# Kernel optimization log

Measured on AMD Instinct MI355X. Metric: run time of the kernel, lower is better.

## Reference

```python
import jax, jax.numpy as jnp
import numpy as np

B, S, D_IN, D_OUT = 4, 2048, 1024, 64
USE_MASK = True

def setup_inputs() -> dict:
    key = jax.random.key(0)
    ks = jax.random.split(key, 6)
    return {
        "inputs_for_keys": jax.random.normal(ks[0], (B, S, D_IN), jnp.float32),
        "inputs_for_values": jax.random.normal(ks[1], (B, S, D_IN), jnp.float32),
        "inputs_for_queries": jax.random.normal(ks[2], (B, S, D_IN), jnp.float32),
        "Weight_Q": jax.random.normal(ks[3], (D_IN, D_OUT), jnp.float32) * 0.02,
        "Weight_K": jax.random.normal(ks[4], (D_IN, D_OUT), jnp.float32) * 0.02,
        "Weight_V": jax.random.normal(ks[5], (D_IN, D_OUT), jnp.float32) * 0.02,
    }

def reference(inputs_for_keys, inputs_for_values, inputs_for_queries, Weight_Q, Weight_K, Weight_V):
    Q = jnp.einsum('bsd,de->bse', inputs_for_queries, Weight_Q)
    K = jnp.einsum('bsd,de->bse', inputs_for_keys, Weight_K)
    V = jnp.einsum('bsd,de->bse', inputs_for_values, Weight_V)
    # scores: [B, S_q, S_k], scaled by sqrt(d_out)
    scores = jnp.einsum('bqe,bke->bqk', Q, K) / np.sqrt(D_OUT).astype(np.float32)
    if USE_MASK:
        # -inf strictly above the diagonal (causal mask), matching
        # transpose(tril(ones*-inf, -1)) in the original.
        q_idx = jnp.arange(S)[:, None]
        k_idx = jnp.arange(S)[None, :]
        scores = jnp.where(k_idx > q_idx, -jnp.inf, scores)
    attn = jax.nn.softmax(scores, axis=-1)
    return jnp.einsum('bqk,bke->bqe', attn, V)
```

## Files before the change

### kernel.cpp

```cpp
#include <hip/hip_runtime.h>
#include <hip/hip_bf16.h>
#include <stdint.h>

typedef __bf16 bf16_t;
typedef __bf16 bf16x8 __attribute__((ext_vector_type(8)));
typedef float f32x4 __attribute__((ext_vector_type(4)));

#define L2E 1.44269504088896340736f

static __device__ __forceinline__ f32x4 mfma16(bf16x8 a, bf16x8 b, f32x4 c) {
  return __builtin_amdgcn_mfma_f32_16x16x32_bf16(a, b, c, 0, 0, 0);
}

__global__ __launch_bounds__(256) void wt_kernel(const float* __restrict__ Wq,
                                                 const float* __restrict__ Wk,
                                                 const float* __restrict__ Wv,
                                                 bf16_t* __restrict__ Wt) {
  int gid = blockIdx.x * 256 + threadIdx.x;
  int proj = gid >> 16;
  int rem = gid & 65535;
  int k = rem >> 6, n = rem & 63;
  const float* W = (proj == 0) ? Wq : (proj == 1) ? Wk : Wv;
  float v = W[rem];
  if (proj == 0) v *= 0.125f;
  Wt[proj * 65536 + n * 1024 + k] = (bf16_t)v;
}

__global__ __launch_bounds__(256, 4) void proj_kernel(
    const float* __restrict__ Xq, const float* __restrict__ Xk, const float* __restrict__ Xv,
    const bf16_t* __restrict__ Wt,
    bf16_t* __restrict__ Qb, bf16_t* __restrict__ Kb, bf16_t* __restrict__ Vt) {
  __shared__ float Msm[4][16][68];
  __shared__ bf16_t Vsm[16][68];

  int tid = threadIdx.x;
  int w = tid >> 6, lane = tid & 63;
  int l15 = lane & 15, g = lane >> 4;
  int bid = blockIdx.x;
  int p = bid >> 9, t = bid & 511;
  int m0 = t * 16;
  const float* X = (p == 0) ? Xq : (p == 1) ? Xk : Xv;

  const float* xk = X + (size_t)(m0 + l15) * 1024 + w * 256 + g * 8;
  const bf16_t* wrow = Wt + p * 65536 + l15 * 1024 + w * 256 + g * 8;

  f32x4 acc[4] = {};

  float4 a0x = *(const float4*)xk;
  float4 a0y = *(const float4*)(xk + 4);
  bf16x8 w0[4], w1[4];
#pragma unroll
  for (int ct = 0; ct < 4; ++ct) w0[ct] = *(const bf16x8*)(wrow + ct * 16384);

  float4 a1x, a1y;
#pragma unroll
  for (int ks = 0; ks < 8; ++ks) {
    if (ks < 7) {
      const float* xn = xk + (ks + 1) * 32;
      a1x = *(const float4*)xn;
      a1y = *(const float4*)(xn + 4);
#pragma unroll
      for (int ct = 0; ct < 4; ++ct)
        w1[ct] = *(const bf16x8*)(wrow + ct * 16384 + (ks + 1) * 32);
    }
    bf16x8 af;
    af[0] = (bf16_t)a0x.x; af[1] = (bf16_t)a0x.y; af[2] = (bf16_t)a0x.z; af[3] = (bf16_t)a0x.w;
    af[4] = (bf16_t)a0y.x; af[5] = (bf16_t)a0y.y; af[6] = (bf16_t)a0y.z; af[7] = (bf16_t)a0y.w;
#pragma unroll
    for (int ct = 0; ct < 4; ++ct) acc[ct] = mfma16(af, w0[ct], acc[ct]);
    a0x = a1x; a0y = a1y;
#pragma unroll
    for (int ct = 0; ct < 4; ++ct) w0[ct] = w1[ct];
  }

#pragma unroll
  for (int ct = 0; ct < 4; ++ct)
#pragma unroll
    for (int r = 0; r < 4; ++r)
      Msm[w][g * 4 + r][ct * 16 + l15] = acc[ct][r];
  __syncthreads();

  int row = tid >> 4, c0 = (tid & 15) * 4;
  f32x4 s = *(const f32x4*)&Msm[0][row][c0];
#pragma unroll
  for (int w2 = 1; w2 < 4; ++w2) {
    f32x4 q = *(const f32x4*)&Msm[w2][row][c0];
    s[0] += q[0]; s[1] += q[1]; s[2] += q[2]; s[3] += q[3];
  }

  if (p < 2) {
    bf16_t* Ob = (p == 0) ? Qb : Kb;
    bf16_t o4[4] = {(bf16_t)s[0], (bf16_t)s[1], (bf16_t)s[2], (bf16_t)s[3]};
    *(uint2*)&Ob[(size_t)(m0 + row) * 64 + c0] = *(const uint2*)o4;
  } else {
#pragma unroll
    for (int i = 0; i < 4; ++i) Vsm[row][c0 + i] = (bf16_t)s[i];
    __syncthreads();
    if (tid < 128) {
      int d = tid >> 1, h = tid & 1;
      int b = t >> 7;
      int s_ = (t & 127) * 16 + h * 8;
      bf16_t tmp[8];
#pragma unroll
      for (int i = 0; i < 8; ++i) tmp[i] = Vsm[h * 8 + i][d];
      *(uint4*)(Vt + ((size_t)(b * 64 + d)) * 2048 + s_) = *(const uint4*)tmp;
    }
  }
}

#define NW 8
__global__ __launch_bounds__(512) void attn_kernel(
    const bf16_t* __restrict__ Qb, const bf16_t* __restrict__ Kb,
    const bf16_t* __restrict__ Vt, float* __restrict__ Out) {
  __shared__ alignas(16) char Psm[NW * 4096];
  __shared__ float accL[NW][32][64];
  __shared__ float mL[NW][32];
  __shared__ float lL[NW][32];

  int b = blockIdx.y;
  int x = blockIdx.x;
  int qt = (b >= 2) ? (63 - x) : x;
  int q0 = qt * 32;
  int tid = threadIdx.x;
  int w = tid >> 6, lane = tid & 63;
  int l15 = lane & 15, g = lane >> 4;
  char* Pw = Psm + w * 4096;

  bf16x8 qf[2][2];
#pragma unroll
  for (int h = 0; h < 2; ++h) {
    size_t qrow = (size_t)(b * 2048 + q0 + h * 16 + l15) * 64;
    qf[h][0] = *(const bf16x8*)(Qb + qrow + g * 8);
    qf[h][1] = *(const bf16x8*)(Qb + qrow + 32 + g * 8);
  }

  float m_run[2][4], l_run[2][4];
  f32x4 acc_o[2][4] = {};
#pragma unroll
  for (int h = 0; h < 2; ++h)
#pragma unroll
    for (int r = 0; r < 4; ++r) { m_run[h][r] = -1e30f; l_run[h][r] = 0.f; }

  int ntiles = (q0 + 95) >> 6;
  const bf16_t* kbase = Kb + (size_t)b * 2048 * 64;
  const bf16_t* vbase = Vt + (size_t)b * 64 * 2048;

  for (int t = w; t < ntiles; t += NW) {
    int kv0 = t * 64;
    f32x4 s[2][4] = {};
#pragma unroll
    for (int ct = 0; ct < 4; ++ct) {
      const bf16_t* kr = kbase + (size_t)(kv0 + ct * 16 + l15) * 64 + g * 8;
      bf16x8 kf0 = *(const bf16x8*)kr;
      bf16x8 kf1 = *(const bf16x8*)(kr + 32);
#pragma unroll
      for (int h = 0; h < 2; ++h) {
        s[h][ct] = mfma16(qf[h][0], kf0, s[h][ct]);
        s[h][ct] = mfma16(qf[h][1], kf1, s[h][ct]);
      }
    }
    if (t == ntiles - 1) {
#pragma unroll
      for (int h = 0; h < 2; ++h)
#pragma unroll
        for (int ct = 0; ct < 4; ++ct)
#pragma unroll
          for (int r = 0; r < 4; ++r) {
            int kg_ = kv0 + ct * 16 + l15;
            int qg_ = q0 + h * 16 + g * 4 + r;
            if (kg_ > qg_) s[h][ct][r] = -1e30f;
          }
    }

#pragma unroll
    for (int h = 0; h < 2; ++h)
#pragma unroll
      for (int r = 0; r < 4; ++r) {
        float mx = fmaxf(fmaxf(s[h][0][r], s[h][1][r]), fmaxf(s[h][2][r], s[h][3][r]));
        mx = fmaxf(mx, __shfl_xor(mx, 1, 64));
        mx = fmaxf(mx, __shfl_xor(mx, 2, 64));
        mx = fmaxf(mx, __shfl_xor(mx, 4, 64));
        mx = fmaxf(mx, __shfl_xor(mx, 8, 64));
        float mnew = fmaxf(m_run[h][r], mx);
        float scale = exp2f((m_run[h][r] - mnew) * L2E);
        m_run[h][r] = mnew;
        float ps = 0.f;
        int qrl = h * 16 + g * 4 + r;
        char* pb = Pw + qrl * 128;
        int swp = (qrl & 7) << 4;
#pragma unroll
        for (int ct = 0; ct < 4; ++ct) {
          float p = exp2f((s[h][ct][r] - mnew) * L2E);
          ps += p;
          *(bf16_t*)(pb + ((ct * 32 + l15 * 2) ^ swp)) = (bf16_t)p;
        }
        ps += __shfl_xor(ps, 1, 64);
        ps += __shfl_xor(ps, 2, 64);
        ps += __shfl_xor(ps, 4, 64);
        ps += __shfl_xor(ps, 8, 64);
        l_run[h][r] = l_run[h][r] * scale + ps;
#pragma unroll
        for (int dt = 0; dt < 4; ++dt) acc_o[h][dt][r] *= scale;
      }

    int swpr = (l15 & 7) << 4;
#pragma unroll
    for (int ks = 0; ks < 2; ++ks) {
      bf16x8 pf0 = *(const bf16x8*)(Pw + l15 * 128 + ((ks * 64 + g * 16) ^ swpr));
      bf16x8 pf1 = *(const bf16x8*)(Pw + (16 + l15) * 128 + ((ks * 64 + g * 16) ^ swpr));
#pragma unroll
      for (int dt = 0; dt < 4; ++dt) {
        const bf16_t* vr = vbase + (size_t)(dt * 16 + l15) * 2048 + kv0 + ks * 32 + g * 8;
        bf16x8 vf = *(const bf16x8*)vr;
        acc_o[0][dt] = mfma16(pf0, vf, acc_o[0][dt]);
        acc_o[1][dt] = mfma16(pf1, vf, acc_o[1][dt]);
      }
    }
  }

  if (l15 == 0) {
#pragma unroll
    for (int h = 0; h < 2; ++h)
#pragma unroll
      for (int r = 0; r < 4; ++r) {
        mL[w][h * 16 + g * 4 + r] = m_run[h][r];
        lL[w][h * 16 + g * 4 + r] = l_run[h][r];
      }
  }
#pragma unroll
  for (int h = 0; h < 2; ++h)
#pragma unroll
    for (int dt = 0; dt < 4; ++dt)
#pragma unroll
      for (int r = 0; r < 4; ++r)
        accL[w][h * 16 + g * 4 + r][dt * 16 + l15] = acc_o[h][dt][r];
  __syncthreads();

  int row = tid >> 4, c0 = (tid & 15) * 4;
  float M = -1e30f;
#pragma unroll
  for (int w2 = 0; w2 < NW; ++w2) M = fmaxf(M, mL[w2][row]);
  float L = 0.f;
  f32x4 o = {0.f, 0.f, 0.f, 0.f};
#pragma unroll
  for (int w2 = 0; w2 < NW; ++w2) {
    float sc = exp2f((mL[w2][row] - M) * L2E);
    L += lL[w2][row] * sc;
    f32x4 a = *(const f32x4*)&accL[w2][row][c0];
    o[0] += sc * a[0]; o[1] += sc * a[1]; o[2] += sc * a[2]; o[3] += sc * a[3];
  }
  float inv = 1.0f / L;
  float4 o4 = {o[0] * inv, o[1] * inv, o[2] * inv, o[3] * inv};
  *(float4*)&Out[(size_t)(b * 2048 + q0 + row) * 64 + c0] = o4;
}

extern "C" void kernel_launch(void* const* d_in, const int* in_sizes, int n_in,
                              void* d_out, int out_size, void* d_ws, size_t ws_size,
                              hipStream_t stream) {
  const float* Xk = (const float*)d_in[0];
  const float* Xv = (const float*)d_in[1];
  const float* Xq = (const float*)d_in[2];
  const float* Wq = (const float*)d_in[3];
  const float* Wk = (const float*)d_in[4];
  const float* Wv = (const float*)d_in[5];
  float* Out = (float*)d_out;

  bf16_t* ws = (bf16_t*)d_ws;
  bf16_t* Qb = ws;
  bf16_t* Kb = ws + 524288;
  bf16_t* Vt = ws + 1048576;
  bf16_t* Wt = ws + 1572864;

  wt_kernel<<<dim3(768), dim3(256), 0, stream>>>(Wq, Wk, Wv, Wt);
  proj_kernel<<<dim3(1536), dim3(256), 0, stream>>>(Xq, Xk, Xv, Wt, Qb, Kb, Vt);
  attn_kernel<<<dim3(64, 4), dim3(512), 0, stream>>>(Qb, Kb, Vt, Out);
}
```

Measured before the change: 65.63 us.

## Stage projection inputs into swizzled LDS via global_load_lds and preload weights

The projection kernel now copies each wave's 16x256 fp32 input slice into a 64KB shared buffer using direct global-to-LDS loads. Each row is read as fully contiguous 1KB segments, replacing the earlier strided per-lane 32-byte reads, and an XOR swizzle avoids bank conflicts when the data is read back from LDS. All weight fragments are loaded into registers up front, replacing the double-buffered software pipeline. The larger LDS footprint and register use cut the occupancy hint from 4 to 2 blocks, and a full vmcnt wait before the MFMA loop removes any overlap between loads and compute.

```diff
diff --git a/kernel.cpp b/kernel.cpp
--- a/kernel.cpp
+++ b/kernel.cpp
@@ -10,6 +10,12 @@
 
 static __device__ __forceinline__ f32x4 mfma16(bf16x8 a, bf16x8 b, f32x4 c) {
   return __builtin_amdgcn_mfma_f32_16x16x32_bf16(a, b, c, 0, 0, 0);
+}
+
+static __device__ __forceinline__ void gload_lds16(const void* g, void* l) {
+  __builtin_amdgcn_global_load_lds(
+      (const __attribute__((address_space(1))) uint32_t*)g,
+      (__attribute__((address_space(3))) uint32_t*)l, 16, 0, 0);
 }
 
 __global__ __launch_bounds__(256) void wt_kernel(const float* __restrict__ Wq,
@@ -26,12 +32,13 @@
   Wt[proj * 65536 + n * 1024 + k] = (bf16_t)v;
 }
 
-__global__ __launch_bounds__(256, 4) void proj_kernel(
+__global__ __launch_bounds__(256, 2) void proj_kernel(
     const float* __restrict__ Xq, const float* __restrict__ Xk, const float* __restrict__ Xv,
     const bf16_t* __restrict__ Wt,
     bf16_t* __restrict__ Qb, bf16_t* __restrict__ Kb, bf16_t* __restrict__ Vt) {
-  __shared__ float Msm[4][16][68];
-  __shared__ bf16_t Vsm[16][68];
+  __shared__ alignas(16) char Xs[65536];
+  float (*Msm)[16][68] = (float(*)[16][68])Xs;
+  bf16_t (*Vsm)[68] = (bf16_t(*)[68])(Xs + 18432);
 
   int tid = threadIdx.x;
   int w = tid >> 6, lane = tid & 63;
@@ -40,39 +47,42 @@
   int p = bid >> 9, t = bid & 511;
   int m0 = t * 16;
   const float* X = (p == 0) ? Xq : (p == 1) ? Xk : Xv;
-
-  const float* xk = X + (size_t)(m0 + l15) * 1024 + w * 256 + g * 8;
+  const char* xb = (const char*)X + (size_t)m0 * 4096;
+  char* Xw = Xs + w * 16384;
+
+  bf16x8 Wf[4][8];
   const bf16_t* wrow = Wt + p * 65536 + l15 * 1024 + w * 256 + g * 8;
+#pragma unroll
+  for (int ct = 0; ct < 4; ++ct)
+#pragma unroll
+    for (int j = 0; j < 8; ++j)
+      Wf[ct][j] = *(const bf16x8*)(wrow + ct * 16384 + j * 32);
+
+#pragma unroll
+  for (int r = 0; r < 16; ++r) {
+    const char* src = xb + (size_t)r * 4096 + w * 1024 + ((lane * 16) ^ (r << 4));
+    gload_lds16(src, Xw + r * 1024);
+  }
+  asm volatile("s_waitcnt vmcnt(0)" ::: "memory");
+  __builtin_amdgcn_sched_barrier(0);
 
   f32x4 acc[4] = {};
-
-  float4 a0x = *(const float4*)xk;
-  float4 a0y = *(const float4*)(xk + 4);
-  bf16x8 w0[4], w1[4];
-#pragma unroll
-  for (int ct = 0; ct < 4; ++ct) w0[ct] = *(const bf16x8*)(wrow + ct * 16384);
-
-  float4 a1x, a1y;
-#pragma unroll
-  for (int ks = 0; ks < 8; ++ks) {
-    if (ks < 7) {
-      const float* xn = xk + (ks + 1) * 32;
-      a1x = *(const float4*)xn;
-      a1y = *(const float4*)(xn + 4);
-#pragma unroll
-      for (int ct = 0; ct < 4; ++ct)
-        w1[ct] = *(const bf16x8*)(wrow + ct * 16384 + (ks + 1) * 32);
-    }
+  const char* bp = Xw + l15 * 1024;
+  int swz = l15 << 4;
+#pragma unroll
+  for (int j = 0; j < 8; ++j) {
+    int b0 = j * 128 + g * 32;
+    float4 u0 = *(const float4*)(bp + (b0 ^ swz));
+    float4 u1 = *(const float4*)(bp + ((b0 + 16) ^ swz));
     bf16x8 af;
-    af[0] = (bf16_t)a0x.x; af[1] = (bf16_t)a0x.y; af[2] = (bf16_t)a0x.z; af[3] = (bf16_t)a0x.w;
-    af[4] = (bf16_t)a0y.x; af[5] = (bf16_t)a0y.y; af[6] = (bf16_t)a0y.z; af[7] = (bf16_t)a0y.w;
-#pragma unroll
-    for (int ct = 0; ct < 4; ++ct) acc[ct] = mfma16(af, w0[ct], acc[ct]);
-    a0x = a1x; a0y = a1y;
-#pragma unroll
-    for (int ct = 0; ct < 4; ++ct) w0[ct] = w1[ct];
-  }
-
+    af[0] = (bf16_t)u0.x; af[1] = (bf16_t)u0.y; af[2] = (bf16_t)u0.z; af[3] = (bf16_t)u0.w;
+    af[4] = (bf16_t)u1.x; af[5] = (bf16_t)u1.y; af[6] = (bf16_t)u1.z; af[7] = (bf16_t)u1.w;
+#pragma unroll
+    for (int ct = 0; ct < 4; ++ct)
+      acc[ct] = mfma16(af, Wf[ct][j], acc[ct]);
+  }
+
+  __syncthreads();
 #pragma unroll
   for (int ct = 0; ct < 4; ++ct)
 #pragma unroll
```

Result: no change. 65.00 us (-1.0%).
